# Kernel optimization log

Measured on AMD Instinct MI355X. Metric: run time of the kernel, lower is better.

The kernel has to match this reference:

```python
import jax, jax.numpy as jnp
import numpy as np

NUM_SPIXELS = 256
N_ITER = 3
TEMP = 1.0


def setup_inputs() -> dict:
    key = jax.random.key(0)
    features = jax.random.normal(key, (4, 16, 256, 256), dtype=jnp.float32)
    return {"features": features}


def reference(features):
    B, C, H, W = features.shape
    dt = features.dtype
    # torch.linspace(0, h-1, h)/h == arange(h)/h
    y = jnp.arange(H, dtype=dt) / H
    x = jnp.arange(W, dtype=dt) / W
    mesh_y, mesh_x = jnp.meshgrid(y, x, indexing='ij')  # each [H, W]
    xy = jnp.stack([mesh_x, mesh_y], axis=0)            # [2, H, W]
    xy_b = jnp.broadcast_to(xy, (B, 2, H, W))

    pixel = jnp.concatenate([features, xy_b], axis=1).reshape(B, C + 2, H * W)
    p = pixel.transpose(0, 2, 1)  # [B, N, D], D = C+2

    s = max(1, int(NUM_SPIXELS ** 0.5))
    # adaptive_avg_pool2d to (s, s); H, W divisible by s -> exact block mean
    def pool(t):
        D = t.shape[1]
        return t.reshape(B, D, s, H // s, s, W // s).mean(axis=(3, 5)).reshape(B, D, s * s)

    centers = jnp.concatenate([pool(features), pool(xy_b)], axis=1)  # [B, D, M]
    c = centers.transpose(0, 2, 1)  # [B, M, D]

    Q = None
    for i in range(N_ITER):
        # Euclidean cdist: ||p||^2 + ||c||^2 - 2 p.c, clipped and sqrt'ed
        d2 = (jnp.sum(p * p, axis=-1)[:, :, None]
              + jnp.sum(c * c, axis=-1)[:, None, :]
              - 2.0 * jnp.einsum('bnd,bmd->bnm', p, c))
        dist = jnp.sqrt(jnp.maximum(d2, 1e-12))  # [B, N, M]
        Q = jax.nn.softmax(-dist * TEMP, axis=-1)
        if i < N_ITER - 1:
            norm = jnp.sum(Q, axis=1)[:, :, None] + 1e-6        # [B, M, 1]
            c = jnp.einsum('bnm,bnd->bmd', Q, p) / norm         # [B, M, D]

    centers_feat = c[:, :, :C].transpose(0, 2, 1)  # [B, C, M]
    return Q, centers_feat
```

## Files before the change

### kernel.cpp

```cpp
#include <hip/hip_runtime.h>
#include <math.h>

#define BB 4
#define CC 16
#define HH 256
#define WW 256
#define NN (HH*WW)
#define MM 256
#define CROW 20
#define PROW 20
#define PIX 32
#define TSUB 4
#define PIXPERBLK (PIX*TSUB)
#define CHUNKS (NN/PIXPERBLK)

typedef float f32x2 __attribute__((ext_vector_type(2)));

__device__ __forceinline__ f32x2 mk2(float a, float b) { f32x2 r; r.x = a; r.y = b; return r; }
__device__ __forceinline__ f32x2 pk_fma(f32x2 a, f32x2 b, f32x2 c) {
    return __builtin_elementwise_fma(a, b, c);
}

__global__ void init_centers(const float* __restrict__ feat, float* __restrict__ cbuf)
{
    const int b    = blockIdx.x >> 8;
    const int m    = blockIdx.x & 255;
    const int lane = threadIdx.x;
    const int sy = m >> 4, sx = m & 15;

    float cvals[16];
#pragma unroll
    for (int d = 0; d < 16; ++d) {
        float v = 0.f;
#pragma unroll
        for (int k = 0; k < 4; ++k) {
            int q  = lane + (k << 6);
            int py = q >> 4, px = q & 15;
            int n  = (sy*16 + py)*WW + sx*16 + px;
            v += feat[((b*CC + d) << 16) + n];
        }
#pragma unroll
        for (int off = 32; off; off >>= 1) v += __shfl_down(v, off);
        cvals[d] = v * (1.f/256.f);
    }
    if (lane == 0) {
        float* row = cbuf + (b*MM + m)*CROW;
        float cn2 = 0.f;
#pragma unroll
        for (int d = 0; d < 16; ++d) { row[d] = cvals[d]; cn2 = fmaf(cvals[d], cvals[d], cn2); }
        float cx = (sx*16 + 7.5f) * (1.f/256.f);
        float cy = (sy*16 + 7.5f) * (1.f/256.f);
        row[16] = cx; row[17] = cy;
        cn2 = fmaf(cx, cx, cn2);
        cn2 = fmaf(cy, cy, cn2);
        row[18] = cn2;
        row[19] = 0.f;
    }
}

__global__ void build_pt(const float* __restrict__ feat, float* __restrict__ ptbuf)
{
    const int b = blockIdx.x >> 8;
    const int n = ((blockIdx.x & 255) << 8) | threadIdx.x;
    float v[16];
#pragma unroll
    for (int d = 0; d < 16; ++d) v[d] = feat[((b*CC + d) << 16) + n];
    float x = (float)(n & 255) * (1.f/256.f);
    float y = (float)(n >> 8) * (1.f/256.f);
    float pn2 = 0.f;
#pragma unroll
    for (int d = 0; d < 16; ++d) pn2 = fmaf(v[d], v[d], pn2);
    pn2 = fmaf(x, x, pn2);
    pn2 = fmaf(y, y, pn2);
    float4* row = reinterpret_cast<float4*>(ptbuf + (size_t)(b*NN + n)*PROW);
    row[0] = make_float4(v[0],  v[1],  v[2],  v[3]);
    row[1] = make_float4(v[4],  v[5],  v[6],  v[7]);
    row[2] = make_float4(v[8],  v[9],  v[10], v[11]);
    row[3] = make_float4(v[12], v[13], v[14], v[15]);
    row[4] = make_float4(x, y, pn2, 1.0f);
}

__global__ __launch_bounds__(256, 3)
void ssn_nf(const float* __restrict__ ptbuf, const float* __restrict__ cbuf,
            float* __restrict__ pp)
{
    __shared__ __align__(16) float pls[PIXPERBLK*PROW];
    __shared__ float ssum_s[TSUB][4][16];
    __shared__ float w_s[TSUB][PIX];
    __shared__ float xfer[128*41];

    const int tid    = threadIdx.x;
    const int b      = blockIdx.x >> 9;
    const int chunk  = blockIdx.x & (CHUNKS-1);
    const int n_base = chunk * PIXPERBLK;
    const int lane   = tid & 63;
    const int wv     = tid >> 6;
    const int mlo    = tid & 127;
    const int pxbase = (tid >> 7) << 4;

    {
        const float4* src = reinterpret_cast<const float4*>(
            ptbuf + (size_t)(b*NN + n_base)*PROW);
#pragma unroll
        for (int k = 0; k < 3; ++k) {
            int f = tid + (k << 8);
            if (f < PIXPERBLK*PROW/4)
                reinterpret_cast<float4*>(pls)[f] = src[f];
        }
    }

    f32x2 cp0[9], cp1[9]; float cn20, cn21;
    {
        const float4* cv = reinterpret_cast<const float4*>(cbuf + (b*MM + mlo)*CROW);
        float4 a0 = cv[0], a1 = cv[1], a2 = cv[2], a3 = cv[3], a4 = cv[4];
        cp0[0]=mk2(a0.x,a0.y); cp0[1]=mk2(a0.z,a0.w);
        cp0[2]=mk2(a1.x,a1.y); cp0[3]=mk2(a1.z,a1.w);
        cp0[4]=mk2(a2.x,a2.y); cp0[5]=mk2(a2.z,a2.w);
        cp0[6]=mk2(a3.x,a3.y); cp0[7]=mk2(a3.z,a3.w);
        cp0[8]=mk2(a4.x,a4.y); cn20=a4.z;
    }
    {
        const float4* cv = reinterpret_cast<const float4*>(cbuf + (b*MM + mlo + 128)*CROW);
        float4 a0 = cv[0], a1 = cv[1], a2 = cv[2], a3 = cv[3], a4 = cv[4];
        cp1[0]=mk2(a0.x,a0.y); cp1[1]=mk2(a0.z,a0.w);
        cp1[2]=mk2(a1.x,a1.y); cp1[3]=mk2(a1.z,a1.w);
        cp1[4]=mk2(a2.x,a2.y); cp1[5]=mk2(a2.z,a2.w);
        cp1[6]=mk2(a3.x,a3.y); cp1[7]=mk2(a3.z,a3.w);
        cp1[8]=mk2(a4.x,a4.y); cn21=a4.z;
    }

    f32x2 acc0[10], acc1[10];
#pragma unroll
    for (int k = 0; k < 10; ++k) { acc0[k] = mk2(0.f,0.f); acc1[k] = mk2(0.f,0.f); }

    const int pxo4 = ((lane&1)<<3) | ((lane&2)<<1) | ((lane&4)>>1) | ((lane&8)>>3);

    __syncthreads();

    for (int t = 0; t < TSUB; ++t) {
        float e0[16], e1[16];
#pragma unroll
        for (int k = 0; k < 16; ++k) {
            const float4* pv = reinterpret_cast<const float4*>(
                &pls[(t*PIX + pxbase + k)*PROW]);
            float4 q0 = pv[0], q1 = pv[1], q2 = pv[2], q3 = pv[3], q4 = pv[4];
            f32x2 u0=mk2(q0.x,q0.y), u1=mk2(q0.z,q0.w), u2=mk2(q1.x,q1.y),
                  u3=mk2(q1.z,q1.w), u4=mk2(q2.x,q2.y), u5=mk2(q2.z,q2.w),
                  u6=mk2(q3.x,q3.y), u7=mk2(q3.z,q3.w), u8=mk2(q4.x,q4.y);
            f32x2 d0 = mk2(0.f,0.f), d1 = mk2(0.f,0.f);
            d0 = pk_fma(u0, cp0[0], d0);  d1 = pk_fma(u0, cp1[0], d1);
            d0 = pk_fma(u1, cp0[1], d0);  d1 = pk_fma(u1, cp1[1], d1);
            d0 = pk_fma(u2, cp0[2], d0);  d1 = pk_fma(u2, cp1[2], d1);
            d0 = pk_fma(u3, cp0[3], d0);  d1 = pk_fma(u3, cp1[3], d1);
            d0 = pk_fma(u4, cp0[4], d0);  d1 = pk_fma(u4, cp1[4], d1);
            d0 = pk_fma(u5, cp0[5], d0);  d1 = pk_fma(u5, cp1[5], d1);
            d0 = pk_fma(u6, cp0[6], d0);  d1 = pk_fma(u6, cp1[6], d1);
            d0 = pk_fma(u7, cp0[7], d0);  d1 = pk_fma(u7, cp1[7], d1);
            d0 = pk_fma(u8, cp0[8], d0);  d1 = pk_fma(u8, cp1[8], d1);
            float d20 = fmaf(-2.f, d0.x + d0.y, q4.z + cn20);
            float d21 = fmaf(-2.f, d1.x + d1.y, q4.z + cn21);
            e0[k] = __expf(-__builtin_amdgcn_sqrtf(fmaxf(d20, 1e-12f)));
            e1[k] = __expf(-__builtin_amdgcn_sqrtf(fmaxf(d21, 1e-12f)));
        }

        float s[8];
        {
            const bool hi = (lane & 1);
#pragma unroll
            for (int k = 0; k < 8; ++k) {
                float a  = e0[k]   + e1[k];
                float bq = e0[k+8] + e1[k+8];
                float recv = __shfl_xor(hi ? a : bq, 1);
                s[k] = (hi ? bq : a) + recv;
            }
        }
#define RS_ROUND(MASK, H) { const bool hi = (lane & (MASK)); \
        _Pragma("unroll") \
        for (int k = 0; k < (H); ++k) { \
            float a = s[k], bq = s[k+(H)]; \
            float recv = __shfl_xor(hi ? a : bq, (MASK)); \
            s[k] = (hi ? bq : a) + recv; } }
        RS_ROUND(2, 4)
        RS_ROUND(4, 2)
        RS_ROUND(8, 1)
#undef RS_ROUND
        s[0] += __shfl_xor(s[0], 16);
        s[0] += __shfl_xor(s[0], 32);
        if (lane < 16) ssum_s[t][wv][pxo4] = s[0];
        __syncthreads();
        if (tid < 32) {
            int h = tid >> 4, p4 = tid & 15;
            w_s[t][tid] = 1.0f / (ssum_s[t][2*h][p4] + ssum_s[t][2*h+1][p4]);
        }
        __syncthreads();

#pragma unroll
        for (int k = 0; k < 16; ++k) {
            const float4* pv = reinterpret_cast<const float4*>(
                &pls[(t*PIX + pxbase + k)*PROW]);
            float4 q0 = pv[0], q1 = pv[1], q2 = pv[2], q3 = pv[3], q4 = pv[4];
            float w = w_s[t][pxbase + k];
            float w0 = e0[k]*w, w1 = e1[k]*w;
            f32x2 ew0 = mk2(w0, w0), ew1 = mk2(w1, w1);
            f32x2 u0=mk2(q0.x,q0.y), u1=mk2(q0.z,q0.w), u2=mk2(q1.x,q1.y),
                  u3=mk2(q1.z,q1.w), u4=mk2(q2.x,q2.y), u5=mk2(q2.z,q2.w),
                  u6=mk2(q3.x,q3.y), u7=mk2(q3.z,q3.w), u8=mk2(q4.x,q4.y),
                  u9=mk2(q4.z,q4.w);
            acc0[0] = pk_fma(ew0, u0, acc0[0]);  acc1[0] = pk_fma(ew1, u0, acc1[0]);
            acc0[1] = pk_fma(ew0, u1, acc0[1]);  acc1[1] = pk_fma(ew1, u1, acc1[1]);
            acc0[2] = pk_fma(ew0, u2, acc0[2]);  acc1[2] = pk_fma(ew1, u2, acc1[2]);
            acc0[3] = pk_fma(ew0, u3, acc0[3]);  acc1[3] = pk_fma(ew1, u3, acc1[3]);
            acc0[4] = pk_fma(ew0, u4, acc0[4]);  acc1[4] = pk_fma(ew1, u4, acc1[4]);
            acc0[5] = pk_fma(ew0, u5, acc0[5]);  acc1[5] = pk_fma(ew1, u5, acc1[5]);
            acc0[6] = pk_fma(ew0, u6, acc0[6]);  acc1[6] = pk_fma(ew1, u6, acc1[6]);
            acc0[7] = pk_fma(ew0, u7, acc0[7]);  acc1[7] = pk_fma(ew1, u7, acc1[7]);
            acc0[8] = pk_fma(ew0, u8, acc0[8]);  acc1[8] = pk_fma(ew1, u8, acc1[8]);
            acc0[9] = pk_fma(ew0, u9, acc0[9]);  acc1[9] = pk_fma(ew1, u9, acc1[9]);
        }
    }

    if (tid >= 128) {
        float* xb = &xfer[(tid - 128)*41];
#pragma unroll
        for (int j = 0; j < 10; ++j) { xb[2*j]    = acc0[j].x; xb[2*j+1]    = acc0[j].y; }
#pragma unroll
        for (int j = 0; j < 10; ++j) { xb[20+2*j] = acc1[j].x; xb[20+2*j+1] = acc1[j].y; }
    }
    __syncthreads();
    if (tid < 128) {
        const float* xb = &xfer[tid*41];
#pragma unroll
        for (int j = 0; j < 10; ++j) { acc0[j].x += xb[2*j];    acc0[j].y += xb[2*j+1]; }
#pragma unroll
        for (int j = 0; j < 10; ++j) { acc1[j].x += xb[20+2*j]; acc1[j].y += xb[20+2*j+1]; }

        float* dst0 = pp + ((size_t)(b*CHUNKS + chunk)*MM + mlo)*PROW;
        float4* v0 = reinterpret_cast<float4*>(dst0);
        v0[0] = make_float4(acc0[0].x, acc0[0].y, acc0[1].x, acc0[1].y);
        v0[1] = make_float4(acc0[2].x, acc0[2].y, acc0[3].x, acc0[3].y);
        v0[2] = make_float4(acc0[4].x, acc0[4].y, acc0[5].x, acc0[5].y);
        v0[3] = make_float4(acc0[6].x, acc0[6].y, acc0[7].x, acc0[7].y);
        v0[4] = make_float4(acc0[8].x, acc0[8].y, acc0[9].y, 0.f);

        float* dst1 = pp + ((size_t)(b*CHUNKS + chunk)*MM + mlo + 128)*PROW;
        float4* v1 = reinterpret_cast<float4*>(dst1);
        v1[0] = make_float4(acc1[0].x, acc1[0].y, acc1[1].x, acc1[1].y);
        v1[1] = make_float4(acc1[2].x, acc1[2].y, acc1[3].x, acc1[3].y);
        v1[2] = make_float4(acc1[4].x, acc1[4].y, acc1[5].x, acc1[5].y);
        v1[3] = make_float4(acc1[6].x, acc1[6].y, acc1[7].x, acc1[7].y);
        v1[4] = make_float4(acc1[8].x, acc1[8].y, acc1[9].y, 0.f);
    }
}

__global__ __launch_bounds__(256, 3)
void ssn_fin(const float* __restrict__ ptbuf, const float* __restrict__ cbuf,
             float* __restrict__ qout)
{
    __shared__ __align__(16) float pls[PIXPERBLK*PROW];
    __shared__ float ssum_s[TSUB][4][PIX];
    __shared__ float w_s[TSUB][PIX];

    const int tid    = threadIdx.x;
    const int b      = blockIdx.x >> 9;
    const int chunk  = blockIdx.x & (CHUNKS-1);
    const int n_base = chunk * PIXPERBLK;
    const int L      = tid & 63;
    const int wv     = tid >> 6;
    const int g      = L & 3;
    const int msub   = L >> 2;
    const int mbase  = wv*64 + msub;

    {
        const float4* src = reinterpret_cast<const float4*>(
            ptbuf + (size_t)(b*NN + n_base)*PROW);
#pragma unroll
        for (int k = 0; k < 3; ++k) {
            int f = tid + (k << 8);
            if (f < PIXPERBLK*PROW/4)
                reinterpret_cast<float4*>(pls)[f] = src[f];
        }
    }

    f32x2 cp[4][9]; float cn2[4];
#pragma unroll
    for (int j = 0; j < 4; ++j) {
        const float4* cv = reinterpret_cast<const float4*>(
            cbuf + (b*MM + mbase + 16*j)*CROW);
        float4 a0 = cv[0], a1 = cv[1], a2 = cv[2], a3 = cv[3], a4 = cv[4];
        cp[j][0]=mk2(a0.x,a0.y); cp[j][1]=mk2(a0.z,a0.w);
        cp[j][2]=mk2(a1.x,a1.y); cp[j][3]=mk2(a1.z,a1.w);
        cp[j][4]=mk2(a2.x,a2.y); cp[j][5]=mk2(a2.z,a2.w);
        cp[j][6]=mk2(a3.x,a3.y); cp[j][7]=mk2(a3.z,a3.w);
        cp[j][8]=mk2(a4.x,a4.y); cn2[j]=a4.z;
    }

    __syncthreads();

    for (int t = 0; t < TSUB; ++t) {
        float e[4][8];
#pragma unroll
        for (int k = 0; k < 8; ++k) {
            const int row = t*PIX + g + 4*k;
            const float4* pv = reinterpret_cast<const float4*>(&pls[row*PROW]);
            float4 q0 = pv[0], q1 = pv[1], q2 = pv[2], q3 = pv[3], q4 = pv[4];
            f32x2 u0=mk2(q0.x,q0.y), u1=mk2(q0.z,q0.w), u2=mk2(q1.x,q1.y),
                  u3=mk2(q1.z,q1.w), u4=mk2(q2.x,q2.y), u5=mk2(q2.z,q2.w),
                  u6=mk2(q3.x,q3.y), u7=mk2(q3.z,q3.w), u8=mk2(q4.x,q4.y);
            f32x2 d0=mk2(0.f,0.f), d1=mk2(0.f,0.f), d2v=mk2(0.f,0.f), d3=mk2(0.f,0.f);
            d0 = pk_fma(u0, cp[0][0], d0); d1 = pk_fma(u0, cp[1][0], d1);
            d2v= pk_fma(u0, cp[2][0], d2v);d3 = pk_fma(u0, cp[3][0], d3);
            d0 = pk_fma(u1, cp[0][1], d0); d1 = pk_fma(u1, cp[1][1], d1);
            d2v= pk_fma(u1, cp[2][1], d2v);d3 = pk_fma(u1, cp[3][1], d3);
            d0 = pk_fma(u2, cp[0][2], d0); d1 = pk_fma(u2, cp[1][2], d1);
            d2v= pk_fma(u2, cp[2][2], d2v);d3 = pk_fma(u2, cp[3][2], d3);
            d0 = pk_fma(u3, cp[0][3], d0); d1 = pk_fma(u3, cp[1][3], d1);
            d2v= pk_fma(u3, cp[2][3], d2v);d3 = pk_fma(u3, cp[3][3], d3);
            d0 = pk_fma(u4, cp[0][4], d0); d1 = pk_fma(u4, cp[1][4], d1);
            d2v= pk_fma(u4, cp[2][4], d2v);d3 = pk_fma(u4, cp[3][4], d3);
            d0 = pk_fma(u5, cp[0][5], d0); d1 = pk_fma(u5, cp[1][5], d1);
            d2v= pk_fma(u5, cp[2][5], d2v);d3 = pk_fma(u5, cp[3][5], d3);
            d0 = pk_fma(u6, cp[0][6], d0); d1 = pk_fma(u6, cp[1][6], d1);
            d2v= pk_fma(u6, cp[2][6], d2v);d3 = pk_fma(u6, cp[3][6], d3);
            d0 = pk_fma(u7, cp[0][7], d0); d1 = pk_fma(u7, cp[1][7], d1);
            d2v= pk_fma(u7, cp[2][7], d2v);d3 = pk_fma(u7, cp[3][7], d3);
            d0 = pk_fma(u8, cp[0][8], d0); d1 = pk_fma(u8, cp[1][8], d1);
            d2v= pk_fma(u8, cp[2][8], d2v);d3 = pk_fma(u8, cp[3][8], d3);
            float s0 = fmaf(-2.f, d0.x + d0.y, q4.z + cn2[0]);
            float s1 = fmaf(-2.f, d1.x + d1.y, q4.z + cn2[1]);
            float s2 = fmaf(-2.f, d2v.x + d2v.y, q4.z + cn2[2]);
            float s3 = fmaf(-2.f, d3.x + d3.y, q4.z + cn2[3]);
            e[0][k] = __expf(-__builtin_amdgcn_sqrtf(fmaxf(s0, 1e-12f)));
            e[1][k] = __expf(-__builtin_amdgcn_sqrtf(fmaxf(s1, 1e-12f)));
            e[2][k] = __expf(-__builtin_amdgcn_sqrtf(fmaxf(s2, 1e-12f)));
            e[3][k] = __expf(-__builtin_amdgcn_sqrtf(fmaxf(s3, 1e-12f)));
        }

        float s[8];
#pragma unroll
        for (int k = 0; k < 8; ++k)
            s[k] = (e[0][k] + e[1][k]) + (e[2][k] + e[3][k]);
#define RS_ROUND(MASK, H) { const bool hi = (L & (MASK)); \
        _Pragma("unroll") \
        for (int k = 0; k < (H); ++k) { \
            float a = s[k], bq = s[k+(H)]; \
            float recv = __shfl_xor(hi ? a : bq, (MASK)); \
            s[k] = (hi ? bq : a) + recv; } }
        RS_ROUND(4, 4)
        RS_ROUND(8, 2)
        RS_ROUND(16, 1)
#undef RS_ROUND
        s[0] += __shfl_xor(s[0], 32);
        {
            const int kown = (((L>>2)&1)<<2) | (((L>>3)&1)<<1) | ((L>>4)&1);
            if (L < 32) ssum_s[t][wv][g + 4*kown] = s[0];
        }
        __syncthreads();
        if (tid < 32) {
            w_s[t][tid] = 1.0f / (ssum_s[t][0][tid] + ssum_s[t][1][tid]
                                + ssum_s[t][2][tid] + ssum_s[t][3][tid]);
        }
        __syncthreads();

#pragma unroll
        for (int k = 0; k < 8; ++k) {
            float w = w_s[t][g + 4*k];
            size_t rowoff = ((size_t)(b*NN + n_base + t*PIX + g + 4*k)) << 8;
#pragma unroll
            for (int j = 0; j < 4; ++j)
                qout[rowoff + mbase + 16*j] = e[j][k] * w;
        }
    }
}

__global__ __launch_bounds__(256)
void reduce_finalize(const float* __restrict__ pp, float* __restrict__ cbuf,
                     float* __restrict__ cfout, int write_cf)
{
    const int b   = blockIdx.x >> 8;
    const int m   = blockIdx.x & 255;
    const int tid = threadIdx.x;
    const int lane = tid & 63, wv = tid >> 6;

    const float4* r0 = reinterpret_cast<const float4*>(
        pp + ((size_t)(b*CHUNKS + tid)*MM + m)*PROW);
    const float4* r1 = reinterpret_cast<const float4*>(
        pp + ((size_t)(b*CHUNKS + tid + 256)*MM + m)*PROW);
    float a[19];
    {
        float4 u0=r0[0], u1=r0[1], u2=r0[2], u3=r0[3], u4=r0[4];
        float4 w0=r1[0], w1=r1[1], w2=r1[2], w3=r1[3], w4=r1[4];
        a[0]=u0.x+w0.x;  a[1]=u0.y+w0.y;  a[2]=u0.z+w0.z;  a[3]=u0.w+w0.w;
        a[4]=u1.x+w1.x;  a[5]=u1.y+w1.y;  a[6]=u1.z+w1.z;  a[7]=u1.w+w1.w;
        a[8]=u2.x+w2.x;  a[9]=u2.y+w2.y;  a[10]=u2.z+w2.z; a[11]=u2.w+w2.w;
        a[12]=u3.x+w3.x; a[13]=u3.y+w3.y; a[14]=u3.z+w3.z; a[15]=u3.w+w3.w;
        a[16]=u4.x+w4.x; a[17]=u4.y+w4.y; a[18]=u4.z+w4.z;
    }
#pragma unroll
    for (int off = 32; off; off >>= 1) {
#pragma unroll
        for (int d = 0; d < 19; ++d) a[d] += __shfl_down(a[d], off);
    }

    __shared__ float red[4][20];
    if (lane == 0) {
#pragma unroll
        for (int d = 0; d < 19; ++d) red[wv][d] = a[d];
    }
    __syncthreads();
    if (tid == 0) {
        float s[19];
#pragma unroll
        for (int d = 0; d < 19; ++d)
            s[d] = red[0][d] + red[1][d] + red[2][d] + red[3][d];
        float den = s[18] + 1e-6f;
        float* row = cbuf + (b*MM + m)*CROW;
        float cn2 = 0.f;
#pragma unroll
        for (int d = 0; d < 18; ++d) {
            float cv = s[d] / den;
            row[d] = cv;
            cn2 = fmaf(cv, cv, cn2);
            if (write_cf && d < 16) cfout[((b*CC + d) << 8) + m] = cv;
        }
        row[18] = cn2;
        row[19] = 0.f;
    }
}

extern "C" void kernel_launch(void* const* d_in, const int* in_sizes, int n_in,
                              void* d_out, int out_size, void* d_ws, size_t ws_size,
                              hipStream_t stream)
{
    const float* feat = (const float*)d_in[0];
    float* dout = (float*)d_out;

    float* cbuf  = (float*)d_ws;
    float* ptbuf = cbuf + 32768;
    float* pp    = ptbuf + (size_t)BB*NN*PROW;

    float* qout  = dout;
    float* cfout = dout + (size_t)BB*NN*MM;

    build_pt<<<dim3(BB*256), dim3(256), 0, stream>>>(feat, ptbuf);
    init_centers<<<dim3(BB*MM), dim3(64), 0, stream>>>(feat, cbuf);

    for (int it = 0; it < 2; ++it) {
        ssn_nf<<<dim3(BB*CHUNKS), dim3(256), 0, stream>>>(ptbuf, cbuf, pp);
        reduce_finalize<<<dim3(BB*MM), dim3(256), 0, stream>>>(pp, cbuf, cfout, it == 1);
    }
    ssn_fin<<<dim3(BB*CHUNKS), dim3(256), 0, stream>>>(ptbuf, cbuf, qout);
}
```

Measured before the change: 275.1 us.

## Remap ssn_fin so each wave owns whole pixel rows and writes float4 Q

In the final softmax kernel, each wave now handles 8 full pixels across all 256 centers, with each lane owning 4 consecutive centers. The softmax row sum is reduced entirely inside the wave with shuffles, which removes the shared-memory partial sums and two block barriers per sub-tile. Q stores become 16-byte vectorized writes of contiguous centers instead of strided scalar stores. The cost is a longer shuffle reduction chain, and all lanes in a wave now read the same pixel rows from LDS (broadcast).

```diff
diff --git a/kernel.cpp b/kernel.cpp
--- a/kernel.cpp
+++ b/kernel.cpp
@@ -21,6 +21,34 @@
     return __builtin_elementwise_fma(a, b, c);
 }
 
+__device__ __forceinline__ void rowdot4(const float* __restrict__ prow,
+                                        const f32x2 (&cp)[4][9], const float (&cn2)[4],
+                                        float (&e)[4])
+{
+    const float4* pv = reinterpret_cast<const float4*>(prow);
+    float4 q0 = pv[0], q1 = pv[1], q2 = pv[2], q3 = pv[3], q4 = pv[4];
+    f32x2 u[9];
+    u[0]=mk2(q0.x,q0.y); u[1]=mk2(q0.z,q0.w); u[2]=mk2(q1.x,q1.y);
+    u[3]=mk2(q1.z,q1.w); u[4]=mk2(q2.x,q2.y); u[5]=mk2(q2.z,q2.w);
+    u[6]=mk2(q3.x,q3.y); u[7]=mk2(q3.z,q3.w); u[8]=mk2(q4.x,q4.y);
+    f32x2 d0=mk2(0.f,0.f), d1=mk2(0.f,0.f), d2=mk2(0.f,0.f), d3=mk2(0.f,0.f);
+#pragma unroll
+    for (int i = 0; i < 9; ++i) {
+        d0 = pk_fma(u[i], cp[0][i], d0);
+        d1 = pk_fma(u[i], cp[1][i], d1);
+        d2 = pk_fma(u[i], cp[2][i], d2);
+        d3 = pk_fma(u[i], cp[3][i], d3);
+    }
+    float s0 = fmaf(-2.f, d0.x + d0.y, q4.z + cn2[0]);
+    float s1 = fmaf(-2.f, d1.x + d1.y, q4.z + cn2[1]);
+    float s2 = fmaf(-2.f, d2.x + d2.y, q4.z + cn2[2]);
+    float s3 = fmaf(-2.f, d3.x + d3.y, q4.z + cn2[3]);
+    e[0] = __expf(-__builtin_amdgcn_sqrtf(fmaxf(s0, 1e-12f)));
+    e[1] = __expf(-__builtin_amdgcn_sqrtf(fmaxf(s1, 1e-12f)));
+    e[2] = __expf(-__builtin_amdgcn_sqrtf(fmaxf(s2, 1e-12f)));
+    e[3] = __expf(-__builtin_amdgcn_sqrtf(fmaxf(s3, 1e-12f)));
+}
+
 __global__ void init_centers(const float* __restrict__ feat, float* __restrict__ cbuf)
 {
     const int b    = blockIdx.x >> 8;
@@ -79,6 +107,25 @@
     row[3] = make_float4(v[12], v[13], v[14], v[15]);
     row[4] = make_float4(x, y, pn2, 1.0f);
 }
+
+#define RS8(L, s) \
+    { const bool hi = ((L) & 1); \
+      _Pragma("unroll") for (int k = 0; k < 4; ++k) { \
+        float a = s[k], bq = s[k+4]; \
+        float recv = __shfl_xor(hi ? a : bq, 1); \
+        s[k] = (hi ? bq : a) + recv; } } \
+    { const bool hi = ((L) & 2); \
+      _Pragma("unroll") for (int k = 0; k < 2; ++k) { \
+        float a = s[k], bq = s[k+2]; \
+        float recv = __shfl_xor(hi ? a : bq, 2); \
+        s[k] = (hi ? bq : a) + recv; } } \
+    { const bool hi = ((L) & 4); \
+      { float a = s[0], bq = s[1]; \
+        float recv = __shfl_xor(hi ? a : bq, 4); \
+        s[0] = (hi ? bq : a) + recv; } } \
+    s[0] += __shfl_xor(s[0], 8); \
+    s[0] += __shfl_xor(s[0], 16); \
+    s[0] += __shfl_xor(s[0], 32);
 
 __global__ __launch_bounds__(256, 3)
 void ssn_nf(const float* __restrict__ ptbuf, const float* __restrict__ cbuf,
@@ -257,8 +304,6 @@
              float* __restrict__ qout)
 {
     __shared__ __align__(16) float pls[PIXPERBLK*PROW];
-    __shared__ float ssum_s[TSUB][4][PIX];
-    __shared__ float w_s[TSUB][PIX];
 
     const int tid    = threadIdx.x;
     const int b      = blockIdx.x >> 9;
@@ -266,9 +311,6 @@
     const int n_base = chunk * PIXPERBLK;
     const int L      = tid & 63;
     const int wv     = tid >> 6;
-    const int g      = L & 3;
-    const int msub   = L >> 2;
-    const int mbase  = wv*64 + msub;
 
     {
         const float4* src = reinterpret_cast<const float4*>(
@@ -285,7 +327,7 @@
 #pragma unroll
     for (int j = 0; j < 4; ++j) {
         const float4* cv = reinterpret_cast<const float4*>(
-            cbuf + (b*MM + mbase + 16*j)*CROW);
+            cbuf + (b*MM + 4*L + j)*CROW);
         float4 a0 = cv[0], a1 = cv[1], a2 = cv[2], a3 = cv[3], a4 = cv[4];
         cp[j][0]=mk2(a0.x,a0.y); cp[j][1]=mk2(a0.z,a0.w);
         cp[j][2]=mk2(a1.x,a1.y); cp[j][3]=mk2(a1.z,a1.w);
@@ -297,77 +339,31 @@
     __syncthreads();
 
     for (int t = 0; t < TSUB; ++t) {
+        const int pxb = t*PIX + wv*8;
+
         float e[4][8];
+        float s[8];
 #pragma unroll
         for (int k = 0; k < 8; ++k) {
-            const int row = t*PIX + g + 4*k;
-            const float4* pv = reinterpret_cast<const float4*>(&pls[row*PROW]);
-            float4 q0 = pv[0], q1 = pv[1], q2 = pv[2], q3 = pv[3], q4 = pv[4];
-            f32x2 u0=mk2(q0.x,q0.y), u1=mk2(q0.z,q0.w), u2=mk2(q1.x,q1.y),
-                  u3=mk2(q1.z,q1.w), u4=mk2(q2.x,q2.y), u5=mk2(q2.z,q2.w),
-                  u6=mk2(q3.x,q3.y), u7=mk2(q3.z,q3.w), u8=mk2(q4.x,q4.y);
-            f32x2 d0=mk2(0.f,0.f), d1=mk2(0.f,0.f), d2v=mk2(0.f,0.f), d3=mk2(0.f,0.f);
-            d0 = pk_fma(u0, cp[0][0], d0); d1 = pk_fma(u0, cp[1][0], d1);
-            d2v= pk_fma(u0, cp[2][0], d2v);d3 = pk_fma(u0, cp[3][0], d3);
-            d0 = pk_fma(u1, cp[0][1], d0); d1 = pk_fma(u1, cp[1][1], d1);
-            d2v= pk_fma(u1, cp[2][1], d2v);d3 = pk_fma(u1, cp[3][1], d3);
-            d0 = pk_fma(u2, cp[0][2], d0); d1 = pk_fma(u2, cp[1][2], d1);
-            d2v= pk_fma(u2, cp[2][2], d2v);d3 = pk_fma(u2, cp[3][2], d3);
-            d0 = pk_fma(u3, cp[0][3], d0); d1 = pk_fma(u3, cp[1][3], d1);
-            d2v= pk_fma(u3, cp[2][3], d2v);d3 = pk_fma(u3, cp[3][3], d3);
-            d0 = pk_fma(u4, cp[0][4], d0); d1 = pk_fma(u4, cp[1][4], d1);
-            d2v= pk_fma(u4, cp[2][4], d2v);d3 = pk_fma(u4, cp[3][4], d3);
-            d0 = pk_fma(u5, cp[0][5], d0); d1 = pk_fma(u5, cp[1][5], d1);
-            d2v= pk_fma(u5, cp[2][5], d2v);d3 = pk_fma(u5, cp[3][5], d3);
-            d0 = pk_fma(u6, cp[0][6], d0); d1 = pk_fma(u6, cp[1][6], d1);
-            d2v= pk_fma(u6, cp[2][6], d2v);d3 = pk_fma(u6, cp[3][6], d3);
-            d0 = pk_fma(u7, cp[0][7], d0); d1 = pk_fma(u7, cp[1][7], d1);
-            d2v= pk_fma(u7, cp[2][7], d2v);d3 = pk_fma(u7, cp[3][7], d3);
-            d0 = pk_fma(u8, cp[0][8], d0); d1 = pk_fma(u8, cp[1][8], d1);
-            d2v= pk_fma(u8, cp[2][8], d2v);d3 = pk_fma(u8, cp[3][8], d3);
-            float s0 = fmaf(-2.f, d0.x + d0.y, q4.z + cn2[0]);
-            float s1 = fmaf(-2.f, d1.x + d1.y, q4.z + cn2[1]);
-            float s2 = fmaf(-2.f, d2v.x + d2v.y, q4.z + cn2[2]);
-            float s3 = fmaf(-2.f, d3.x + d3.y, q4.z + cn2[3]);
-            e[0][k] = __expf(-__builtin_amdgcn_sqrtf(fmaxf(s0, 1e-12f)));
-            e[1][k] = __expf(-__builtin_amdgcn_sqrtf(fmaxf(s1, 1e-12f)));
-            e[2][k] = __expf(-__builtin_amdgcn_sqrtf(fmaxf(s2, 1e-12f)));
-            e[3][k] = __expf(-__builtin_amdgcn_sqrtf(fmaxf(s3, 1e-12f)));
-        }
-
-        float s[8];
+            float ek[4];
+            rowdot4(&pls[(pxb + k)*PROW], cp, cn2, ek);
+            e[0][k] = ek[0]; e[1][k] = ek[1]; e[2][k] = ek[2]; e[3][k] = ek[3];
+            s[k] = (ek[0] + ek[1]) + (ek[2] + ek[3]);
+        }
+
+        RS8(L, s)
+        float wr = 1.0f / s[0];
+        float w[8];
 #pragma unroll
         for (int k = 0; k < 8; ++k)
-            s[k] = (e[0][k] + e[1][k]) + (e[2][k] + e[3][k]);
-#define RS_ROUND(MASK, H) { const bool hi = (L & (MASK)); \
-        _Pragma("unroll") \
-        for (int k = 0; k < (H); ++k) { \
-            float a = s[k], bq = s[k+(H)]; \
-            float recv = __shfl_xor(hi ? a : bq, (MASK)); \
-            s[k] = (hi ? bq : a) + recv; } }
-        RS_ROUND(4, 4)
-        RS_ROUND(8, 2)
-        RS_ROUND(16, 1)
-#undef RS_ROUND
-        s[0] += __shfl_xor(s[0], 32);
-        {
-            const int kown = (((L>>2)&1)<<2) | (((L>>3)&1)<<1) | ((L>>4)&1);
-            if (L < 32) ssum_s[t][wv][g + 4*kown] = s[0];
-        }
-        __syncthreads();
-        if (tid < 32) {
-            w_s[t][tid] = 1.0f / (ssum_s[t][0][tid] + ssum_s[t][1][tid]
-                                + ssum_s[t][2][tid] + ssum_s[t][3][tid]);
-        }
-        __syncthreads();
+            w[k] = __shfl(wr, ((k&1)<<2) | (k&2) | ((k>>2)&1));
 
 #pragma unroll
         for (int k = 0; k < 8; ++k) {
-            float w = w_s[t][g + 4*k];
-            size_t rowoff = ((size_t)(b*NN + n_base + t*PIX + g + 4*k)) << 8;
-#pragma unroll
-            for (int j = 0; j < 4; ++j)
-                qout[rowoff + mbase + 16*j] = e[j][k] * w;
+            size_t rowoff = ((size_t)(b*NN + n_base + pxb + k)) << 8;
+            float4 qv = make_float4(e[0][k]*w[k], e[1][k]*w[k],
+                                    e[2][k]*w[k], e[3][k]*w[k]);
+            *reinterpret_cast<float4*>(qout + rowoff + 4*L) = qv;
         }
     }
 }
```

After: 270.1 us. No clear change (-1.8%).
